# Kernel optimization log

Hardware: AMD Instinct MI355X
Metric: run time of the kernel (lower is better)

The kernel has to match this reference:

```python
import jax, jax.numpy as jnp
import numpy as np

N_HEAD = 12

def setup_inputs() -> dict:
    key = jax.random.key(0)
    ks = jax.random.split(key, 5)
    B, T, C = 4, 2048, 768
    x = jax.random.normal(ks[0], (B, T, C), dtype=jnp.float32)
    s_in = 1.0 / np.sqrt(C)
    W_qkv = jax.random.normal(ks[1], (C, 3 * C), dtype=jnp.float32) * s_in
    b_qkv = jnp.zeros((3 * C,), dtype=jnp.float32)
    W_proj = jax.random.normal(ks[2], (C, C), dtype=jnp.float32) * s_in
    b_proj = jnp.zeros((C,), dtype=jnp.float32)
    return {"x": x, "W_qkv": W_qkv, "b_qkv": b_qkv, "W_proj": W_proj, "b_proj": b_proj}


def reference(x, W_qkv, b_qkv, W_proj, b_proj):
    B, T, C = x.shape
    H = N_HEAD
    D = C // H  # head dim
    qkv = x @ W_qkv + b_qkv                      # [B,T,3C]
    q, k, v = jnp.split(qkv, 3, axis=-1)
    # [B,T,C] -> [B,H,T,D]
    q = q.reshape(B, T, H, D).transpose(0, 2, 1, 3)
    k = k.reshape(B, T, H, D).transpose(0, 2, 1, 3)
    v = v.reshape(B, T, H, D).transpose(0, 2, 1, 3)
    att = jnp.einsum("bhqd,bhkd->bhqk", q, k) / jnp.sqrt(jnp.asarray(D, x.dtype))
    causal = jnp.tril(jnp.ones((T, T), dtype=bool))
    att = jnp.where(causal, att, jnp.asarray(-jnp.inf, att.dtype))
    att = jax.nn.softmax(att, axis=-1)
    y = jnp.einsum("bhqk,bhkd->bhqd", att, v)    # [B,H,T,D]
    y = y.transpose(0, 2, 1, 3).reshape(B, T, C)
    return y @ W_proj + b_proj
```

## Files before the change

### kernel.cpp

```cpp
#include <hip/hip_runtime.h>
#include <hip/hip_bf16.h>

typedef __bf16 bf16x8 __attribute__((ext_vector_type(8)));
typedef float f32x4 __attribute__((ext_vector_type(4)));
typedef unsigned int u32x4 __attribute__((ext_vector_type(4)));
typedef unsigned int u32x2 __attribute__((ext_vector_type(2)));
typedef unsigned short u16;
typedef unsigned long long u64;

__device__ __forceinline__ u16 f2bf(float f) {
  unsigned u = __builtin_bit_cast(unsigned, f);
  u += 0x7FFFu + ((u >> 16) & 1u);
  return (u16)(u >> 16);
}
__device__ __forceinline__ unsigned cvtpk(float a, float b) {
  float2 f; f.x = a; f.y = b;
  __hip_bfloat162 h = __float22bfloat162_rn(f);
  unsigned u;
  __builtin_memcpy(&u, &h, 4);
  return u;
}

__device__ __forceinline__ void gll16(const u16* g, u16* l) {
  __builtin_amdgcn_global_load_lds(
      (const __attribute__((address_space(1))) unsigned int*)g,
      (__attribute__((address_space(3))) unsigned int*)l, 16, 0, 0);
}

__global__ void cast_x_kernel(const float* __restrict__ in, u16* __restrict__ out, int n4) {
  int i = blockIdx.x * blockDim.x + threadIdx.x;
  if (i >= n4) return;
  f32x4 v = *(const f32x4*)(in + (size_t)i * 4);
  u32x2 pk;
  pk[0] = cvtpk(v[0], v[1]);
  pk[1] = cvtpk(v[2], v[3]);
  *(u32x2*)(out + (size_t)i * 4) = pk;
}

__global__ void transpose_cast_kernel(const float* __restrict__ W, u16* __restrict__ WT, int K, int N) {
  __shared__ float tile[32][33];
  int c0 = blockIdx.x * 32, r0 = blockIdx.y * 32;
  int tx = threadIdx.x & 31, tg = threadIdx.x >> 5;
#pragma unroll
  for (int i = 0; i < 4; ++i) {
    int r = tg + i * 8;
    tile[r][tx] = W[(size_t)(r0 + r) * N + c0 + tx];
  }
  __syncthreads();
#pragma unroll
  for (int i = 0; i < 4; ++i) {
    int r = tg + i * 8;
    WT[(size_t)(c0 + r) * K + r0 + tx] = f2bf(tile[tx][r]);
  }
}

__global__ __launch_bounds__(256, 4) void gemm_qkv_kernel(
    const u16* __restrict__ A, const u16* __restrict__ BT, const float* __restrict__ bias,
    u16* __restrict__ Qb, u16* __restrict__ Kb, u16* __restrict__ Vt) {
  constexpr int K = 768;
  __shared__ u16 Asm[2][128 * 32];
  __shared__ u16 Bsm[2][128 * 32];
  const int tid = threadIdx.x;
  const int w = tid >> 6, lane = tid & 63;
  const int l15 = lane & 15, quad = lane >> 4;
  const int srow = tid >> 2, scol = (tid & 3) * 8;
  const int m0 = blockIdx.y * 128, n0 = blockIdx.x * 128;
  const u16* Ag = A + (size_t)(m0 + srow) * K + scol;
  const u16* Bg = BT + (size_t)(n0 + srow) * K + scol;
  const int mw = (w >> 1) * 64, nw = (w & 1) * 64;
  f32x4 acc[4][4];
#pragma unroll
  for (int i = 0; i < 4; ++i)
#pragma unroll
    for (int j = 0; j < 4; ++j) acc[i][j] = {0.f, 0.f, 0.f, 0.f};
  for (int k0 = 0; k0 < K; k0 += 64) {
    __syncthreads();
#pragma unroll
    for (int h = 0; h < 2; ++h)
#pragma unroll
      for (int rb = 0; rb < 2; ++rb) {
        gll16(Ag + (size_t)rb * 64 * K + k0 + h * 32, &Asm[h][(rb * 64 + w * 16) * 32]);
        gll16(Bg + (size_t)rb * 64 * K + k0 + h * 32, &Bsm[h][(rb * 64 + w * 16) * 32]);
      }
    __syncthreads();
#pragma unroll
    for (int h = 0; h < 2; ++h) {
      bf16x8 af[4], bfj[4];
#pragma unroll
      for (int i = 0; i < 4; ++i) af[i] = *(const bf16x8*)&Asm[h][(mw + i * 16 + l15) * 32 + quad * 8];
#pragma unroll
      for (int j = 0; j < 4; ++j) bfj[j] = *(const bf16x8*)&Bsm[h][(nw + j * 16 + l15) * 32 + quad * 8];
#pragma unroll
      for (int i = 0; i < 4; ++i)
#pragma unroll
        for (int j = 0; j < 4; ++j)
          acc[i][j] = __builtin_amdgcn_mfma_f32_16x16x32_bf16(af[i], bfj[j], acc[i][j], 0, 0, 0);
    }
  }
  const int sec = blockIdx.x / 6;
  const int nbase = n0 - sec * 768;
#pragma unroll
  for (int j = 0; j < 4; ++j) {
    const int nloc = nbase + nw + j * 16 + l15;
    const float bv = bias[sec * 768 + nloc];
    const int h = nloc >> 6, d = nloc & 63;
#pragma unroll
    for (int i = 0; i < 4; ++i) {
      const int m = m0 + mw + i * 16 + quad * 4;
      const int bb = m >> 11, trow = m & 2047;
      if (sec == 2) {
        u32x2 pk;
        pk[0] = cvtpk(acc[i][j][0] + bv, acc[i][j][1] + bv);
        pk[1] = cvtpk(acc[i][j][2] + bv, acc[i][j][3] + bv);
        *(u32x2*)(Vt + (size_t)((bb * 12 + h) * 64 + d) * 2048 + trow) = pk;
      } else {
        u16* dst = (sec == 0) ? Qb : Kb;
        const float scl = (sec == 0) ? 0.125f * 1.44269504f : 1.0f;
#pragma unroll
        for (int r = 0; r < 4; ++r)
          dst[(size_t)((bb * 12 + h) * 2048 + trow + r) * 64 + d] = f2bf((acc[i][j][r] + bv) * scl);
      }
    }
  }
}

__global__ __launch_bounds__(256, 4) void gemm_proj_kernel(
    const u16* __restrict__ A, const u16* __restrict__ BT, const float* __restrict__ bias,
    float* __restrict__ out) {
  constexpr int K = 768;
  __shared__ u16 Asm[2][64 * 32];
  __shared__ u16 Bsm[2][128 * 32];
  const int tid = threadIdx.x;
  const int w = tid >> 6, lane = tid & 63;
  const int l15 = lane & 15, quad = lane >> 4;
  const int srow = tid >> 2, scol = (tid & 3) * 8;
  const int m0 = blockIdx.y * 64, n0 = blockIdx.x * 128;
  const u16* Ag = A + (size_t)(m0 + srow) * K + scol;
  const u16* Bg = BT + (size_t)(n0 + srow) * K + scol;
  const int mw = (w >> 1) * 32, nw = (w & 1) * 64;
  f32x4 acc[2][4];
#pragma unroll
  for (int i = 0; i < 2; ++i)
#pragma unroll
    for (int j = 0; j < 4; ++j) acc[i][j] = {0.f, 0.f, 0.f, 0.f};
  for (int k0 = 0; k0 < K; k0 += 64) {
    __syncthreads();
#pragma unroll
    for (int h = 0; h < 2; ++h) {
      gll16(Ag + k0 + h * 32, &Asm[h][(w * 16) * 32]);
#pragma unroll
      for (int rb = 0; rb < 2; ++rb)
        gll16(Bg + (size_t)rb * 64 * K + k0 + h * 32, &Bsm[h][(rb * 64 + w * 16) * 32]);
    }
    __syncthreads();
#pragma unroll
    for (int h = 0; h < 2; ++h) {
      bf16x8 af[2], bfj[4];
#pragma unroll
      for (int i = 0; i < 2; ++i) af[i] = *(const bf16x8*)&Asm[h][(mw + i * 16 + l15) * 32 + quad * 8];
#pragma unroll
      for (int j = 0; j < 4; ++j) bfj[j] = *(const bf16x8*)&Bsm[h][(nw + j * 16 + l15) * 32 + quad * 8];
#pragma unroll
      for (int i = 0; i < 2; ++i)
#pragma unroll
        for (int j = 0; j < 4; ++j)
          acc[i][j] = __builtin_amdgcn_mfma_f32_16x16x32_bf16(af[i], bfj[j], acc[i][j], 0, 0, 0);
    }
  }
#pragma unroll
  for (int j = 0; j < 4; ++j) {
    const int n = n0 + nw + j * 16 + l15;
    const float bv = bias[n];
#pragma unroll
    for (int i = 0; i < 2; ++i) {
      const int m = m0 + mw + i * 16 + quad * 4;
#pragma unroll
      for (int r = 0; r < 4; ++r) out[(size_t)(m + r) * 768 + n] = acc[i][j][r] + bv;
    }
  }
}

__global__ __launch_bounds__(256) void attn_split_kernel(
    const u16* __restrict__ Qg, const u16* __restrict__ Kg, const u16* __restrict__ Vtg,
    u16* __restrict__ Yb, float* __restrict__ Opart, float* __restrict__ lpart) {
  constexpr int T = 2048, D = 64;
  constexpr int LDP = 72;
  constexpr float MBOUND = 20.0f;
  __shared__ u16 Ks[64 * LDP];
  __shared__ u16 VTs[64 * LDP];
  __shared__ u16 Ps[4 * 16 * LDP];
  const int s = 79 - blockIdx.x;
  const int bh = blockIdx.y;
  int qt, c;
  if (s < 8) { qt = s; c = 0; }
  else if (s < 24) { qt = 8 + ((s - 8) >> 1); c = (s - 8) & 1; }
  else if (s < 48) { int u = s - 24; int q3 = u / 3; qt = 16 + q3; c = u - 3 * q3; }
  else { int u = s - 48; qt = 24 + (u >> 2); c = u & 3; }
  const int niter = min(8, qt + 1 - 8 * c);
  const int tid = threadIdx.x;
  const int w = tid >> 6, lane = tid & 63;
  const int l15 = lane & 15, quad = lane >> 4;
  const int srow = tid >> 2, scol = (tid & 3) * 16;
  const u16* Kp = Kg + (size_t)bh * T * D;
  const u16* VTp = Vtg + (size_t)bh * D * T;
  u16* pw = &Ps[(w * 16) * LDP];

  const int qq = qt * 64 + w * 16 + l15;
  const u16* qrow = Qg + ((size_t)bh * T + qq) * D;
  const bf16x8 qfa = *(const bf16x8*)(qrow + quad * 8);
  const bf16x8 qfb = *(const bf16x8*)(qrow + 32 + quad * 8);

  f32x4 o[4] = {{0,0,0,0},{0,0,0,0},{0,0,0,0},{0,0,0,0}};
  float lv = 0.f;

  int ktg = c * 8;
  u32x4 kA = *(const u32x4*)(Kp + (size_t)(ktg * 64 + srow) * D + scol);
  u32x4 kB = *(const u32x4*)(Kp + (size_t)(ktg * 64 + srow) * D + scol + 8);
  u32x4 vA = *(const u32x4*)(VTp + (size_t)srow * T + ktg * 64 + scol);
  u32x4 vB = *(const u32x4*)(VTp + (size_t)srow * T + ktg * 64 + scol + 8);

  for (int j = 0; j < niter; ++j) {
    ktg = c * 8 + j;
    __syncthreads();
    *(u32x4*)&Ks[srow * LDP + scol] = kA;
    *(u32x4*)&Ks[srow * LDP + scol + 8] = kB;
    *(u32x4*)&VTs[srow * LDP + scol] = vA;
    *(u32x4*)&VTs[srow * LDP + scol + 8] = vB;
    __syncthreads();
    if (j + 1 < niter) {
      const int k1 = (ktg + 1) * 64;
      kA = *(const u32x4*)(Kp + (size_t)(k1 + srow) * D + scol);
      kB = *(const u32x4*)(Kp + (size_t)(k1 + srow) * D + scol + 8);
      vA = *(const u32x4*)(VTp + (size_t)srow * T + k1 + scol);
      vB = *(const u32x4*)(VTp + (size_t)srow * T + k1 + scol + 8);
    }
    f32x4 sA[4] = {{0,0,0,0},{0,0,0,0},{0,0,0,0},{0,0,0,0}};
#pragma unroll
    for (int t = 0; t < 4; ++t) {
      const bf16x8 kf0 = *(const bf16x8*)&Ks[(t * 16 + l15) * LDP + quad * 8];
      const bf16x8 kf1 = *(const bf16x8*)&Ks[(t * 16 + l15) * LDP + 32 + quad * 8];
      sA[t] = __builtin_amdgcn_mfma_f32_16x16x32_bf16(kf0, qfa, sA[t], 0, 0, 0);
      sA[t] = __builtin_amdgcn_mfma_f32_16x16x32_bf16(kf1, qfb, sA[t], 0, 0, 0);
    }
    if (ktg == qt) {
      const int k0 = ktg * 64;
#pragma unroll
      for (int t = 0; t < 4; ++t)
#pragma unroll
        for (int r = 0; r < 4; ++r)
          if (k0 + t * 16 + quad * 4 + r > qq) sA[t][r] = -1e30f;
    }
#pragma unroll
    for (int t = 0; t < 4; ++t) {
      float e0 = __builtin_amdgcn_exp2f(sA[t][0] - MBOUND);
      float e1 = __builtin_amdgcn_exp2f(sA[t][1] - MBOUND);
      float e2 = __builtin_amdgcn_exp2f(sA[t][2] - MBOUND);
      float e3 = __builtin_amdgcn_exp2f(sA[t][3] - MBOUND);
      lv += (e0 + e1) + (e2 + e3);
      u32x2 pk;
      pk[0] = cvtpk(e0, e1);
      pk[1] = cvtpk(e2, e3);
      *(u32x2*)&pw[l15 * LDP + t * 16 + quad * 4] = pk;
    }
    const bf16x8 pa = *(const bf16x8*)&pw[l15 * LDP + quad * 8];
    const bf16x8 pb = *(const bf16x8*)&pw[l15 * LDP + 32 + quad * 8];
#pragma unroll
    for (int t = 0; t < 4; ++t) {
      const bf16x8 vf0 = *(const bf16x8*)&VTs[(t * 16 + l15) * LDP + quad * 8];
      const bf16x8 vf1 = *(const bf16x8*)&VTs[(t * 16 + l15) * LDP + 32 + quad * 8];
      o[t] = __builtin_amdgcn_mfma_f32_16x16x32_bf16(vf0, pa, o[t], 0, 0, 0);
      o[t] = __builtin_amdgcn_mfma_f32_16x16x32_bf16(vf1, pb, o[t], 0, 0, 0);
    }
  }
  lv += __shfl_xor(lv, 16);
  lv += __shfl_xor(lv, 32);
  if (qt <= 7) {
    const float inv = 1.f / lv;
    const int bidx = bh / 12, hidx = bh % 12;
    u16* y = Yb + ((size_t)bidx * T + qq) * 768 + hidx * 64;
#pragma unroll
    for (int t = 0; t < 4; ++t) {
      u32x2 pk;
      pk[0] = cvtpk(o[t][0] * inv, o[t][1] * inv);
      pk[1] = cvtpk(o[t][2] * inv, o[t][3] * inv);
      *(u32x2*)(y + t * 16 + quad * 4) = pk;
    }
  } else {
    const size_t pidx = (size_t)bh * 80 + s;
    float* Op = Opart + pidx * 4096 + (size_t)(w * 16 + l15) * 64;
#pragma unroll
    for (int t = 0; t < 4; ++t) *(f32x4*)(Op + t * 16 + quad * 4) = o[t];
    if (quad == 0) lpart[pidx * 64 + w * 16 + l15] = lv;
  }
}

__global__ __launch_bounds__(256) void attn_combine_kernel(
    const float* __restrict__ Opart, const float* __restrict__ lpart, u16* __restrict__ Yb) {
  constexpr int T = 2048;
  const int qt = 8 + blockIdx.x;
  const int bh = blockIdx.y;
  const int nch = (qt < 16) ? 2 : (qt < 24) ? 3 : 4;
  const int off = (qt < 16) ? 8 + (qt - 8) * 2 : (qt < 24) ? 24 + (qt - 16) * 3 : 48 + (qt - 24) * 4;
  const size_t base = (size_t)bh * 80 + off;
  const int tid = threadIdx.x;
  const int q = tid >> 2, db = (tid & 3) * 16;
  f32x4 o[4] = {{0,0,0,0},{0,0,0,0},{0,0,0,0},{0,0,0,0}};
  float l = 0.f;
  for (int cc = 0; cc < nch; ++cc) {
    const float* Op = Opart + (base + cc) * 4096 + (size_t)q * 64 + db;
#pragma unroll
    for (int v = 0; v < 4; ++v) o[v] += *(const f32x4*)(Op + v * 4);
    l += lpart[(base + cc) * 64 + q];
  }
  const float inv = 1.f / l;
  const int bidx = bh / 12, hidx = bh % 12;
  u16* y = Yb + ((size_t)bidx * T + qt * 64 + q) * 768 + hidx * 64 + db;
  u32x4 pk;
  pk[0] = cvtpk(o[0][0] * inv, o[0][1] * inv);
  pk[1] = cvtpk(o[0][2] * inv, o[0][3] * inv);
  pk[2] = cvtpk(o[1][0] * inv, o[1][1] * inv);
  pk[3] = cvtpk(o[1][2] * inv, o[1][3] * inv);
  *(u32x4*)y = pk;
  pk[0] = cvtpk(o[2][0] * inv, o[2][1] * inv);
  pk[1] = cvtpk(o[2][2] * inv, o[2][3] * inv);
  pk[2] = cvtpk(o[3][0] * inv, o[3][1] * inv);
  pk[3] = cvtpk(o[3][2] * inv, o[3][3] * inv);
  *(u32x4*)(y + 8) = pk;
}

__global__ __launch_bounds__(256) void attn_kernel(
    const u16* __restrict__ Qg, const u16* __restrict__ Kg, const u16* __restrict__ Vtg,
    u16* __restrict__ Yb) {
  constexpr int T = 2048, D = 64;
  constexpr int LDP = 72;
  constexpr float MBOUND = 20.0f;
  __shared__ u16 Ks[64 * LDP];
  __shared__ u16 VTs[64 * LDP];
  __shared__ u16 Ps[4 * 32 * LDP];
  const int qb = 15 - blockIdx.x;
  const int bh = blockIdx.y;
  const int Q0 = qb * 128;
  const int bidx = bh / 12, hidx = bh % 12;
  const int tid = threadIdx.x;
  const int w = tid >> 6, lane = tid & 63;
  const int l15 = lane & 15, quad = lane >> 4;
  const int srow = tid >> 2, scol = (tid & 3) * 16;
  const u16* Kp = Kg + (size_t)bh * T * D;
  const u16* VTp = Vtg + (size_t)bh * D * T;
  u16* pw0 = &Ps[(w * 32) * LDP];
  u16* pw1 = &Ps[(w * 32 + 16) * LDP];
  const u16* qrow0 = Qg + ((size_t)bh * T + Q0 + w * 16 + l15) * D;
  const bf16x8 qf0a = *(const bf16x8*)(qrow0 + quad * 8);
  const bf16x8 qf0b = *(const bf16x8*)(qrow0 + 32 + quad * 8);
  const bf16x8 qf1a = *(const bf16x8*)(qrow0 + (size_t)64 * D + quad * 8);
  const bf16x8 qf1b = *(const bf16x8*)(qrow0 + (size_t)64 * D + 32 + quad * 8);
  const int qq0 = Q0 + w * 16 + l15, qq1 = qq0 + 64;
  f32x4 o0[4] = {{0,0,0,0},{0,0,0,0},{0,0,0,0},{0,0,0,0}};
  f32x4 o1[4] = {{0,0,0,0},{0,0,0,0},{0,0,0,0},{0,0,0,0}};
  float l0v = 0.f, l1v = 0.f;
  const int nkt = 2 * qb + 2;
  u32x4 kA = *(const u32x4*)(Kp + (size_t)srow * D + scol);
  u32x4 kB = *(const u32x4*)(Kp + (size_t)srow * D + scol + 8);
  u32x4 vA = *(const u32x4*)(VTp + (size_t)srow * T + scol);
  u32x4 vB = *(const u32x4*)(VTp + (size_t)srow * T + scol + 8);
  for (int kt = 0; kt < nkt; ++kt) {
    __syncthreads();
    *(u32x4*)&Ks[srow * LDP + scol] = kA;
    *(u32x4*)&Ks[srow * LDP + scol + 8] = kB;
    *(u32x4*)&VTs[srow * LDP + scol] = vA;
    *(u32x4*)&VTs[srow * LDP + scol + 8] = vB;
    __syncthreads();
    if (kt + 1 < nkt) {
      const int k1 = (kt + 1) * 64;
      kA = *(const u32x4*)(Kp + (size_t)(k1 + srow) * D + scol);
      kB = *(const u32x4*)(Kp + (size_t)(k1 + srow) * D + scol + 8);
      vA = *(const u32x4*)(VTp + (size_t)srow * T + k1 + scol);
      vB = *(const u32x4*)(VTp + (size_t)srow * T + k1 + scol + 8);
    }
    const int k0 = kt * 64;
    const bool g0a = (kt <= 2 * qb);
    f32x4 s0[4] = {{0,0,0,0},{0,0,0,0},{0,0,0,0},{0,0,0,0}};
    f32x4 s1[4] = {{0,0,0,0},{0,0,0,0},{0,0,0,0},{0,0,0,0}};
#pragma unroll
    for (int t = 0; t < 4; ++t) {
      const bf16x8 kf0 = *(const bf16x8*)&Ks[(t * 16 + l15) * LDP + quad * 8];
      const bf16x8 kf1 = *(const bf16x8*)&Ks[(t * 16 + l15) * LDP + 32 + quad * 8];
      s0[t] = __builtin_amdgcn_mfma_f32_16x16x32_bf16(kf0, qf0a, s0[t], 0, 0, 0);
      s0[t] = __builtin_amdgcn_mfma_f32_16x16x32_bf16(kf1, qf0b, s0[t], 0, 0, 0);
      s1[t] = __builtin_amdgcn_mfma_f32_16x16x32_bf16(kf0, qf1a, s1[t], 0, 0, 0);
      s1[t] = __builtin_amdgcn_mfma_f32_16x16x32_bf16(kf1, qf1b, s1[t], 0, 0, 0);
    }
    if (g0a) {
      if (kt == 2 * qb) {
#pragma unroll
        for (int t = 0; t < 4; ++t)
#pragma unroll
          for (int r = 0; r < 4; ++r)
            if (k0 + t * 16 + quad * 4 + r > qq0) s0[t][r] = -1e30f;
      }
#pragma unroll
      for (int t = 0; t < 4; ++t) {
        float e0 = __builtin_amdgcn_exp2f(s0[t][0] - MBOUND);
        float e1 = __builtin_amdgcn_exp2f(s0[t][1] - MBOUND);
        float e2 = __builtin_amdgcn_exp2f(s0[t][2] - MBOUND);
        float e3 = __builtin_amdgcn_exp2f(s0[t][3] - MBOUND);
        l0v += (e0 + e1) + (e2 + e3);
        u32x2 pk;
        pk[0] = cvtpk(e0, e1);
        pk[1] = cvtpk(e2, e3);
        *(u32x2*)&pw0[l15 * LDP + t * 16 + quad * 4] = pk;
      }
    }
    {
      if (kt == 2 * qb + 1) {
#pragma unroll
        for (int t = 0; t < 4; ++t)
#pragma unroll
          for (int r = 0; r < 4; ++r)
            if (k0 + t * 16 + quad * 4 + r > qq1) s1[t][r] = -1e30f;
      }
#pragma unroll
      for (int t = 0; t < 4; ++t) {
        float e0 = __builtin_amdgcn_exp2f(s1[t][0] - MBOUND);
        float e1 = __builtin_amdgcn_exp2f(s1[t][1] - MBOUND);
        float e2 = __builtin_amdgcn_exp2f(s1[t][2] - MBOUND);
        float e3 = __builtin_amdgcn_exp2f(s1[t][3] - MBOUND);
        l1v += (e0 + e1) + (e2 + e3);
        u32x2 pk;
        pk[0] = cvtpk(e0, e1);
        pk[1] = cvtpk(e2, e3);
        *(u32x2*)&pw1[l15 * LDP + t * 16 + quad * 4] = pk;
      }
    }
    const bf16x8 p0a = *(const bf16x8*)&pw0[l15 * LDP + quad * 8];
    const bf16x8 p0b = *(const bf16x8*)&pw0[l15 * LDP + 32 + quad * 8];
    const bf16x8 p1a = *(const bf16x8*)&pw1[l15 * LDP + quad * 8];
    const bf16x8 p1b = *(const bf16x8*)&pw1[l15 * LDP + 32 + quad * 8];
#pragma unroll
    for (int t = 0; t < 4; ++t) {
      const bf16x8 vf0 = *(const bf16x8*)&VTs[(t * 16 + l15) * LDP + quad * 8];
      const bf16x8 vf1 = *(const bf16x8*)&VTs[(t * 16 + l15) * LDP + 32 + quad * 8];
      if (g0a) {
        o0[t] = __builtin_amdgcn_mfma_f32_16x16x32_bf16(vf0, p0a, o0[t], 0, 0, 0);
        o0[t] = __builtin_amdgcn_mfma_f32_16x16x32_bf16(vf1, p0b, o0[t], 0, 0, 0);
      }
      o1[t] = __builtin_amdgcn_mfma_f32_16x16x32_bf16(vf0, p1a, o1[t], 0, 0, 0);
      o1[t] = __builtin_amdgcn_mfma_f32_16x16x32_bf16(vf1, p1b, o1[t], 0, 0, 0);
    }
  }
  l0v += __shfl_xor(l0v, 16); l0v += __shfl_xor(l0v, 32);
  l1v += __shfl_xor(l1v, 16); l1v += __shfl_xor(l1v, 32);
  const float inv0 = 1.f / l0v, inv1 = 1.f / l1v;
  u16* y0 = Yb + ((size_t)bidx * T + qq0) * 768 + hidx * 64;
  u16* y1 = Yb + ((size_t)bidx * T + qq1) * 768 + hidx * 64;
#pragma unroll
  for (int t = 0; t < 4; ++t) {
    u32x2 pk0, pk1;
    pk0[0] = cvtpk(o0[t][0] * inv0, o0[t][1] * inv0);
    pk0[1] = cvtpk(o0[t][2] * inv0, o0[t][3] * inv0);
    pk1[0] = cvtpk(o1[t][0] * inv1, o1[t][1] * inv1);
    pk1[1] = cvtpk(o1[t][2] * inv1, o1[t][3] * inv1);
    *(u32x2*)(y0 + t * 16 + quad * 4) = pk0;
    *(u32x2*)(y1 + t * 16 + quad * 4) = pk1;
  }
}

extern "C" void kernel_launch(void* const* d_in, const int* in_sizes, int n_in,
                              void* d_out, int out_size, void* d_ws, size_t ws_size,
                              hipStream_t stream) {
  const float* x = (const float*)d_in[0];
  const float* W_qkv = (const float*)d_in[1];
  const float* b_qkv = (const float*)d_in[2];
  const float* W_proj = (const float*)d_in[3];
  const float* b_proj = (const float*)d_in[4];
  float* out = (float*)d_out;

  constexpr size_t MC = (size_t)8192 * 768;
  u16* xb = (u16*)d_ws;
  u16* Qb = xb + MC;
  u16* Kb = Qb + MC;
  u16* Vt = Kb + MC;
  u16* Yb = Vt + MC;
  u16* WqkvT = Yb + MC;
  u16* WprojT = WqkvT + (size_t)2304 * 768;
  constexpr size_t BASE_U16 = 5 * MC + (size_t)2304 * 768 + (size_t)768 * 768;
  float* Opart = (float*)((u16*)d_ws + BASE_U16);
  float* lpart = Opart + (size_t)3840 * 4096;
  constexpr size_t NEED = BASE_U16 * 2 + ((size_t)3840 * 4096 + (size_t)3840 * 64) * 4;
  const bool use_split = (ws_size >= NEED);

  cast_x_kernel<<<6291456 / (4 * 256), 256, 0, stream>>>(x, xb, 6291456 / 4);
  transpose_cast_kernel<<<dim3(2304 / 32, 768 / 32), 256, 0, stream>>>(W_qkv, WqkvT, 768, 2304);
  transpose_cast_kernel<<<dim3(768 / 32, 768 / 32), 256, 0, stream>>>(W_proj, WprojT, 768, 768);
  gemm_qkv_kernel<<<dim3(18, 64), 256, 0, stream>>>(xb, WqkvT, b_qkv, Qb, Kb, Vt);
  if (use_split) {
    attn_split_kernel<<<dim3(80, 48), 256, 0, stream>>>(Qb, Kb, Vt, Yb, Opart, lpart);
    attn_combine_kernel<<<dim3(24, 48), 256, 0, stream>>>(Opart, lpart, Yb);
  } else {
    attn_kernel<<<dim3(16, 48), 256, 0, stream>>>(Qb, Kb, Vt, Yb);
  }
  gemm_proj_kernel<<<dim3(6, 128), 256, 0, stream>>>(Yb, WprojT, b_proj, out);
}
```

Measured before the change: 232.2 us.

## Replace LDS round-trip for P with permlane32 swap and permuted V layout

The softmax probabilities P are now rearranged into the MFMA B-operand layout in registers using permlane32_swap, which removes the per-wave shared-memory buffer and its store/load round-trip. To make the register permutation line up, the V^T tile is written to LDS with a matching column permutation. The max-bound subtraction is folded into the score accumulator's initial value, saving one subtract per element. This depends on the permutation being exactly consistent between P and V. A mismatch would give wrong results rather than a slowdown.

```diff
diff --git a/kernel.cpp b/kernel.cpp
--- a/kernel.cpp
+++ b/kernel.cpp
@@ -5,6 +5,7 @@
 typedef float f32x4 __attribute__((ext_vector_type(4)));
 typedef unsigned int u32x4 __attribute__((ext_vector_type(4)));
 typedef unsigned int u32x2 __attribute__((ext_vector_type(2)));
+typedef int i32x2 __attribute__((ext_vector_type(2)));
 typedef unsigned short u16;
 typedef unsigned long long u64;
 
@@ -19,6 +20,12 @@
   unsigned u;
   __builtin_memcpy(&u, &h, 4);
   return u;
+}
+
+__device__ __forceinline__ void plswap(unsigned &a, unsigned &b) {
+  i32x2 r = __builtin_amdgcn_permlane32_swap((int)a, (int)b, false, false);
+  a = (unsigned)r[0];
+  b = (unsigned)r[1];
 }
 
 __device__ __forceinline__ void gll16(const u16* g, u16* l) {
@@ -188,7 +195,6 @@
   constexpr float MBOUND = 20.0f;
   __shared__ u16 Ks[64 * LDP];
   __shared__ u16 VTs[64 * LDP];
-  __shared__ u16 Ps[4 * 16 * LDP];
   const int s = 79 - blockIdx.x;
   const int bh = blockIdx.y;
   int qt, c;
@@ -203,7 +209,6 @@
   const int srow = tid >> 2, scol = (tid & 3) * 16;
   const u16* Kp = Kg + (size_t)bh * T * D;
   const u16* VTp = Vtg + (size_t)bh * D * T;
-  u16* pw = &Ps[(w * 16) * LDP];
 
   const int qq = qt * 64 + w * 16 + l15;
   const u16* qrow = Qg + ((size_t)bh * T + qq) * D;
@@ -224,8 +229,16 @@
     __syncthreads();
     *(u32x4*)&Ks[srow * LDP + scol] = kA;
     *(u32x4*)&Ks[srow * LDP + scol + 8] = kB;
-    *(u32x4*)&VTs[srow * LDP + scol] = vA;
-    *(u32x4*)&VTs[srow * LDP + scol + 8] = vB;
+    {
+      u32x2 t0; t0[0] = vA[0]; t0[1] = vA[1];
+      u32x2 t1; t1[0] = vA[2]; t1[1] = vA[3];
+      u32x2 t2; t2[0] = vB[0]; t2[1] = vB[1];
+      u32x2 t3; t3[0] = vB[2]; t3[1] = vB[3];
+      *(u32x2*)&VTs[srow * LDP + scol] = t0;
+      *(u32x2*)&VTs[srow * LDP + scol + 8] = t1;
+      *(u32x2*)&VTs[srow * LDP + scol + 4] = t2;
+      *(u32x2*)&VTs[srow * LDP + scol + 12] = t3;
+    }
     __syncthreads();
     if (j + 1 < niter) {
       const int k1 = (ktg + 1) * 64;
@@ -234,7 +247,9 @@
       vA = *(const u32x4*)(VTp + (size_t)srow * T + k1 + scol);
       vB = *(const u32x4*)(VTp + (size_t)srow * T + k1 + scol + 8);
     }
-    f32x4 sA[4] = {{0,0,0,0},{0,0,0,0},{0,0,0,0},{0,0,0,0}};
+    f32x4 sA[4];
+#pragma unroll
+    for (int t = 0; t < 4; ++t) sA[t] = {-MBOUND, -MBOUND, -MBOUND, -MBOUND};
 #pragma unroll
     for (int t = 0; t < 4; ++t) {
       const bf16x8 kf0 = *(const bf16x8*)&Ks[(t * 16 + l15) * LDP + quad * 8];
@@ -250,20 +265,25 @@
         for (int r = 0; r < 4; ++r)
           if (k0 + t * 16 + quad * 4 + r > qq) sA[t][r] = -1e30f;
     }
+    unsigned W[4][2];
 #pragma unroll
     for (int t = 0; t < 4; ++t) {
-      float e0 = __builtin_amdgcn_exp2f(sA[t][0] - MBOUND);
-      float e1 = __builtin_amdgcn_exp2f(sA[t][1] - MBOUND);
-      float e2 = __builtin_amdgcn_exp2f(sA[t][2] - MBOUND);
-      float e3 = __builtin_amdgcn_exp2f(sA[t][3] - MBOUND);
+      float e0 = __builtin_amdgcn_exp2f(sA[t][0]);
+      float e1 = __builtin_amdgcn_exp2f(sA[t][1]);
+      float e2 = __builtin_amdgcn_exp2f(sA[t][2]);
+      float e3 = __builtin_amdgcn_exp2f(sA[t][3]);
       lv += (e0 + e1) + (e2 + e3);
-      u32x2 pk;
-      pk[0] = cvtpk(e0, e1);
-      pk[1] = cvtpk(e2, e3);
-      *(u32x2*)&pw[l15 * LDP + t * 16 + quad * 4] = pk;
-    }
-    const bf16x8 pa = *(const bf16x8*)&pw[l15 * LDP + quad * 8];
-    const bf16x8 pb = *(const bf16x8*)&pw[l15 * LDP + 32 + quad * 8];
+      W[t][0] = cvtpk(e0, e1);
+      W[t][1] = cvtpk(e2, e3);
+    }
+    plswap(W[0][0], W[1][0]);
+    plswap(W[0][1], W[1][1]);
+    plswap(W[2][0], W[3][0]);
+    plswap(W[2][1], W[3][1]);
+    u32x4 paw; paw[0] = W[0][0]; paw[1] = W[0][1]; paw[2] = W[1][0]; paw[3] = W[1][1];
+    u32x4 pbw; pbw[0] = W[2][0]; pbw[1] = W[2][1]; pbw[2] = W[3][0]; pbw[3] = W[3][1];
+    const bf16x8 pa = __builtin_bit_cast(bf16x8, paw);
+    const bf16x8 pb = __builtin_bit_cast(bf16x8, pbw);
 #pragma unroll
     for (int t = 0; t < 4; ++t) {
       const bf16x8 vf0 = *(const bf16x8*)&VTs[(t * 16 + l15) * LDP + quad * 8];
```

Result: no change. 231.4 us (-0.3%).
